# Kernel tuning notes

Hardware: AMD Instinct MI355X
Metric: run time of the kernel (lower is better)

The kernel has to match this reference:

```python
import jax, jax.numpy as jnp
import numpy as np

TAU = 0.75

def normalize_W(W):
    n = jnp.linalg.norm(W)
    n = jax.nn.relu(n - 1.0) + 1.0
    return W / n

def setup_inputs() -> dict:
    key = jax.random.key(0)
    ks = jax.random.split(key, 14)
    C_in, C_out, K = 64, 128, 3
    B, L = 32, 4096
    nh = 64
    chunk_in_d = C_out * K            # 384
    D = C_in * (K + 2 * (C_out // C_in))  # 448
    r = lambda k, shp, s=1.0: jax.random.normal(k, shp, dtype=jnp.float32) * s
    W = normalize_W(r(ks[4], (D, 32)))
    return {
        "x": r(ks[0], (B, C_in, L)),
        "conv_weight": r(ks[1], (C_out, C_in, K), 0.1),
        "bias_param": r(ks[2], (C_out,), 0.1),
        "grads": r(ks[3], (C_out * C_in * K,), 0.1),
        "W": W,
        "ctrl_w": r(ks[5], (nh, chunk_in_d), 0.05),
        "ctrl_b": r(ks[6], (nh,), 0.05),
        "cw_w": r(ks[7], (K, nh), 0.05),
        "cw_b": r(ks[8], (K,), 0.05),
        "cb_w": r(ks[9], (C_out // C_in, nh), 0.05),
        "cb_b": r(ks[10], (C_out // C_in,), 0.05),
        "cf_w": r(ks[11], (C_out // C_in, nh), 0.05),
        "cf_b": r(ks[12], (C_out // C_in,), 0.05),
        "trigger": 1,
    }

def fw_chunks(grads, W, ctrl_w, ctrl_b, cw_w, cw_b, cb_w, cb_b, cf_w, cf_b, trigger, n_chunks):
    g = grads.reshape(n_chunks, -1)                    # (C_in, C_out*K)
    rep = jax.nn.silu(g @ ctrl_w.T + ctrl_b)           # (C_in, nh)
    w = rep @ cw_w.T + cw_b                            # (C_in, K)
    b = rep @ cb_w.T + cb_b                            # (C_in, C_out/C_in)
    f = rep @ cf_w.T + cf_b                            # (C_in, C_out/C_in)
    q = jnp.concatenate([w.ravel(), b.ravel(), f.ravel()])  # (D,)  first call: no q_ema
    W_upd = W
    if trigger == 1:  # codebook attention / top-k / scatter-EMA path
        dim = w.shape[0]
        att = jax.nn.softmax(q @ W / 0.5)              # (32,)
        v, idx = jax.lax.top_k(att, 2)
        ww = W[:, idx]                                 # (D, 2)
        old_w = ww @ idx.astype(jnp.float32)[:, None]  # (D, 1) -- indices used as weights, as in source
        s_att = jnp.zeros((att.shape[0],), jnp.float32).at[idx].set(v)
        W_contrib = old_w @ s_att[None, :]             # (D, 32)
        mask = jnp.ones(W.shape, jnp.float32).at[:, idx].set(TAU)
        W_upd = normalize_W(mask * W + (1.0 - mask) * W_contrib)
        nw, nb, nf = w.shape[1], b.shape[1], f.shape[1]
        o_w = old_w[: nw * dim]
        o_b = old_w[nw * dim : (nw + nb) * dim]
        o_f = old_w[-nf * dim :]
        w = TAU * w + (1.0 - TAU) * o_w.reshape(w.shape)
        b = TAU * b + (1.0 - TAU) * o_b.reshape(b.shape)
        f = TAU * f + (1.0 - TAU) * o_f.reshape(f.shape)
    f = f.reshape(-1)[None, :, None]                   # (1, C_out, 1)
    return w[None], b.reshape(-1), f, W_upd

def reference(x, conv_weight, bias_param, grads, W, ctrl_w, ctrl_b, cw_w, cw_b, cb_w, cb_b, cf_w, cf_b, trigger):
    n_chunks = conv_weight.shape[1]  # in_channels
    w, b, f, W_upd = fw_chunks(grads, W, ctrl_w, ctrl_b, cw_w, cw_b, cb_w, cb_b, cf_w, cf_b, trigger, n_chunks)
    cw = conv_weight * w                               # (C_out, C_in, K)
    pad = ((conv_weight.shape[2] - 1) * 1 + 1) // 2    # receptive_field // 2
    conv_out = jax.lax.conv_general_dilated(
        x, cw, window_strides=(1,), padding=[(pad, pad)], rhs_dilation=(1,),
        dimension_numbers=("NCH", "OIH", "NCH"))
    conv_out = conv_out + (bias_param * b)[None, :, None]
    out = f * conv_out                                 # (B, C_out, L)
    return out, W_upd
```

## Files before the change

kernel.cpp:

```cpp
#include <hip/hip_runtime.h>
#include <hip/hip_bf16.h>
#include <math.h>

#define TAU 0.75f

typedef _Float16 half8 __attribute__((ext_vector_type(8)));
typedef float    f32x4 __attribute__((ext_vector_type(4)));

#define LDS_BARRIER() do {                                   \
    asm volatile("s_waitcnt lgkmcnt(0)" ::: "memory");       \
    __builtin_amdgcn_s_barrier();                            \
    asm volatile("" ::: "memory");                           \
} while (0)

#define SWZ(row) ((((row) >> 3) & 7) << 3)

#define WS_Q     0
#define WS_NORM2 448
#define WS_SCALE 449
#define WS_V01   450
#define WS_I01   452
#define WS_WQ    456
#define WS_FSC   648
#define WS_BADD  776
#define WS_OW    904
#define WS_WF16  1352

__global__ __launch_bounds__(256) void k1_rep_q(
    const float* __restrict__ grads, const float* __restrict__ ctrl_w,
    const float* __restrict__ ctrl_b,
    const float* __restrict__ cw_w, const float* __restrict__ cw_b,
    const float* __restrict__ cb_w, const float* __restrict__ cb_b,
    const float* __restrict__ cf_w, const float* __restrict__ cf_b,
    const float* __restrict__ W, float* __restrict__ ws)
{
    const int t = threadIdx.x;
    if (blockIdx.x == 64) {
        __shared__ float red[256];
        float ss = 0.f;
        for (int e = t; e < 3584; e += 256) {
            const float4 w4 = ((const float4*)W)[e];
            ss += w4.x * w4.x + w4.y * w4.y + w4.z * w4.z + w4.w * w4.w;
        }
        red[t] = ss; __syncthreads();
        for (int s = 128; s > 0; s >>= 1) { if (t < s) red[t] += red[t + s]; __syncthreads(); }
        if (t == 0) ws[WS_NORM2] = red[0];
        return;
    }
    const int c = blockIdx.x;
    __shared__ float gS[384];
    __shared__ float repS[64];
    if (t < 96) ((float4*)gS)[t] = ((const float4*)(grads + c * 384))[t];
    __syncthreads();
    {
        const int h = t >> 2, sub = t & 3;
        const float4* wa = (const float4*)(ctrl_w + h * 384) + sub * 24;
        const float4* ga = (const float4*)gS + sub * 24;
        float dot = 0.f;
        #pragma unroll
        for (int d = 0; d < 24; d++) {
            const float4 a = ga[d], b = wa[d];
            dot += a.x * b.x + a.y * b.y + a.z * b.z + a.w * b.w;
        }
        dot += __shfl_xor(dot, 1);
        dot += __shfl_xor(dot, 2);
        if (sub == 0) {
            const float z = dot + ctrl_b[h];
            repS[h] = z / (1.f + expf(-z));
        }
    }
    __syncthreads();
    if (t < 7) {
        const float* wv; float bias; int e;
        if (t < 3)      { wv = cw_w + t * 64;       bias = cw_b[t];     e = 3 * c + t; }
        else if (t < 5) { const int j = t - 3; wv = cb_w + j * 64; bias = cb_b[j]; e = 192 + 2 * c + j; }
        else            { const int j = t - 5; wv = cf_w + j * 64; bias = cf_b[j]; e = 320 + 2 * c + j; }
        float dot = 0.f;
        #pragma unroll 8
        for (int h = 0; h < 64; h++) dot += repS[h] * wv[h];
        ws[WS_Q + e] = dot + bias;
    }
}

__global__ __launch_bounds__(256) void k2_small(
    const float* __restrict__ W, const float* __restrict__ bias_param,
    const int* __restrict__ trigger, float* __restrict__ ws)
{
    __shared__ float qS[448], owS[448], sS[32], sW[4][32], red[256];
    __shared__ int   idxS[2];
    __shared__ float vS[2];
    const int t = threadIdx.x;
    const int wv = t >> 6, lane = t & 63;
    const int trig = trigger[0];

    for (int e = t; e < 448; e += 256) qS[e] = ws[WS_Q + e];
    __syncthreads();

    {
        const int m = lane & 31, half = lane >> 5;
        float s = 0.f;
        const int base = wv * 112;
        #pragma unroll 4
        for (int it = 0; it < 56; it++) {
            const int d = base + it * 2 + half;
            s += qS[d] * W[d * 32 + m];
        }
        s += __shfl_xor(s, 32);
        if (lane < 32) sW[wv][lane] = s;
    }
    __syncthreads();
    if (t < 32) sS[t] = 2.f * (sW[0][t] + sW[1][t] + sW[2][t] + sW[3][t]);
    __syncthreads();
    if (t == 0) {
        float mx = sS[0];
        for (int m = 1; m < 32; m++) mx = fmaxf(mx, sS[m]);
        float sum = 0.f; float att[32];
        for (int m = 0; m < 32; m++) { att[m] = expf(sS[m] - mx); sum += att[m]; }
        const float inv = 1.f / sum;
        int i0 = 0; float v0 = att[0];
        for (int m = 1; m < 32; m++) if (att[m] > v0) { v0 = att[m]; i0 = m; }
        int i1 = -1; float v1 = -1.f;
        for (int m = 0; m < 32; m++) { if (m == i0) continue; if (att[m] > v1) { v1 = att[m]; i1 = m; } }
        idxS[0] = i0; idxS[1] = i1; vS[0] = v0 * inv; vS[1] = v1 * inv;
    }
    __syncthreads();
    const int i0 = idxS[0], i1 = idxS[1];
    const float v0 = vS[0], v1 = vS[1];

    float corr = 0.f;
    for (int d = t; d < 448; d += 256) {
        const float w0 = W[d * 32 + i0], w1 = W[d * 32 + i1];
        const float ow = (trig == 1) ? (w0 * (float)i0 + w1 * (float)i1) : 0.f;
        owS[d] = ow;
        if (trig == 1) {
            const float n0 = TAU * w0 + 0.25f * ow * v0;
            const float n1 = TAU * w1 + 0.25f * ow * v1;
            corr += n0 * n0 - w0 * w0 + n1 * n1 - w1 * w1;
        }
    }
    red[t] = corr; __syncthreads();
    for (int s = 128; s > 0; s >>= 1) { if (t < s) red[t] += red[t + s]; __syncthreads(); }
    if (t == 0) {
        const float n = sqrtf(fmaxf(ws[WS_NORM2] + red[0], 0.f));
        ws[WS_SCALE] = 1.f / fmaxf(n, 1.f);
        ws[WS_V01] = v0; ws[WS_V01 + 1] = v1;
        ((int*)ws)[WS_I01] = i0; ((int*)ws)[WS_I01 + 1] = i1;
    }

    if (t < 192) ws[WS_WQ + t] = (trig == 1) ? (TAU * qS[t] + 0.25f * owS[t]) : qS[t];
    for (int o = t; o < 128; o += 256) {
        float bb = qS[192 + o], ff = qS[320 + o];
        if (trig == 1) {
            bb = TAU * bb + 0.25f * owS[192 + o];
            ff = TAU * ff + 0.25f * owS[320 + o];
        }
        ws[WS_FSC + o]  = ff;
        ws[WS_BADD + o] = ff * bias_param[o] * bb;
    }
    for (int d = t; d < 448; d += 256) ws[WS_OW + d] = owS[d];
}

__global__ __launch_bounds__(256) void k3_finalize(
    const float* __restrict__ W, const float* __restrict__ conv_weight,
    const int* __restrict__ trigger, const float* __restrict__ ws,
    float* __restrict__ W_out, _Float16* __restrict__ wf_out)
{
    const int g = blockIdx.x * 256 + threadIdx.x;
    const int trig = trigger[0];
    if (g < 14336) {
        const float wv = W[g];
        float wn = wv;
        if (trig == 1) {
            const int d = g >> 5, m = g & 31;
            const int i0 = ((const int*)ws)[WS_I01], i1 = ((const int*)ws)[WS_I01 + 1];
            if (m == i0)      wn = TAU * wv + 0.25f * ws[WS_OW + d] * ws[WS_V01];
            else if (m == i1) wn = TAU * wv + 0.25f * ws[WS_OW + d] * ws[WS_V01 + 1];
            wn *= ws[WS_SCALE];
        }
        W_out[g] = wn;
    } else {
        const int e2 = g - 14336;
        const int o   = e2 / 192;
        const int rem = e2 - o * 192;
        const int i   = rem / 3;
        const int kk  = rem - i * 3;
        wf_out[(kk * 128 + o) * 64 + i] =
            (_Float16)(conv_weight[e2] * ws[WS_WQ + rem] * ws[WS_FSC + o]);
    }
}

__global__ __launch_bounds__(256, 2) void conv_mfma(
    const float* __restrict__ x, const _Float16* __restrict__ wf,
    const float* __restrict__ badd, float* __restrict__ out)
{
    __shared__ __align__(16) _Float16 xs[2][66 * 72];

    const int t     = threadIdx.x;
    const int wv    = t >> 6;
    const int lane  = t & 63;
    const int lrow  = lane & 15;
    const int lgrp  = lane >> 4;
    const int b     = blockIdx.x >> 4;
    const int lbase = (blockIdx.x & 15) * 256;
    const int obase = wv * 32;

    const float* xb = x + (size_t)b * 64 * 4096;
    const int ci = t & 3;
    const int ir = t >> 2;
    const int ei = t & 63;
    const int side = (t >> 6) & 1;

    half8 Wf[2][2][3];
    #pragma unroll
    for (int of = 0; of < 2; of++)
        #pragma unroll
        for (int ch = 0; ch < 2; ch++)
            #pragma unroll
            for (int kk = 0; kk < 3; kk++)
                Wf[of][ch][kk] = *(const half8*)(wf + ((kk * 128 + obase + of * 16 + lrow) * 64 + ch * 32 + lgrp * 8));

    float ba_[2];
    #pragma unroll
    for (int of = 0; of < 2; of++)
        ba_[of] = badd[obase + of * 16 + lrow];

    float4 xrA[4], xrB[4];
    float  xeA = 0.f, xeB = 0.f;

#define STAGE_LOAD(xr, xe, lb) do {                                          \
    _Pragma("unroll")                                                        \
    for (int j = 0; j < 4; j++)                                              \
        (xr)[j] = *(const float4*)(xb + (size_t)ir * 4096 + (lb) + ci * 16 + j * 4); \
    (xe) = 0.f;                                                              \
    if (t < 128) {                                                           \
        const int l_ = side ? ((lb) + 64) : ((lb) - 1);                      \
        if (l_ >= 0 && l_ < 4096) (xe) = xb[(size_t)ei * 4096 + l_];         \
    }                                                                        \
} while (0)

#define STAGE_WRITE(buf, xr, xe) do {                                        \
    _Pragma("unroll")                                                        \
    for (int j = 0; j < 4; j++) {                                            \
        const int r0_ = ci * 16 + j * 4 + 1;                                 \
        (buf)[(r0_ + 0) * 72 + (ir ^ SWZ(r0_ + 0))] = (_Float16)(xr)[j].x;   \
        (buf)[(r0_ + 1) * 72 + (ir ^ SWZ(r0_ + 1))] = (_Float16)(xr)[j].y;   \
        (buf)[(r0_ + 2) * 72 + (ir ^ SWZ(r0_ + 2))] = (_Float16)(xr)[j].z;   \
        (buf)[(r0_ + 3) * 72 + (ir ^ SWZ(r0_ + 3))] = (_Float16)(xr)[j].w;   \
    }                                                                        \
    if (t < 128) {                                                           \
        const int re_ = side ? 65 : 0;                                       \
        (buf)[re_ * 72 + (ei ^ SWZ(re_))] = (_Float16)(xe);                  \
    }                                                                        \
} while (0)

#define COMPUTE_STORE(buf, lb) do {                                          \
    f32x4 acc[2][4];                                                         \
    _Pragma("unroll")                                                        \
    for (int of = 0; of < 2; of++)                                           \
        _Pragma("unroll")                                                    \
        for (int lf = 0; lf < 4; lf++) acc[of][lf] = (f32x4)0.f;             \
    _Pragma("unroll")                                                        \
    for (int ch = 0; ch < 2; ch++) {                                         \
        _Pragma("unroll")                                                    \
        for (int kk = 0; kk < 3; kk++) {                                     \
            half8 Xf[4];                                                     \
            _Pragma("unroll")                                                \
            for (int lf = 0; lf < 4; lf++) {                                 \
                const int rr_ = lf * 16 + lrow + kk;                         \
                Xf[lf] = *(const half8*)((buf) + rr_ * 72 + ((ch * 32 + lgrp * 8) ^ SWZ(rr_))); \
            }                                                                \
            _Pragma("unroll")                                                \
            for (int of = 0; of < 2; of++)                                   \
                _Pragma("unroll")                                            \
                for (int lf = 0; lf < 4; lf++)                               \
                    acc[of][lf] = __builtin_amdgcn_mfma_f32_16x16x32_f16(Xf[lf], Wf[of][ch][kk], acc[of][lf], 0, 0, 0); \
        }                                                                    \
    }                                                                        \
    _Pragma("unroll")                                                        \
    for (int of = 0; of < 2; of++) {                                         \
        const int o_ = obase + of * 16 + lrow;                               \
        float* orow_ = out + ((size_t)(b * 128 + o_)) * 4096 + (lb) + lgrp * 4; \
        _Pragma("unroll")                                                    \
        for (int lf = 0; lf < 4; lf++) {                                     \
            float4 r_;                                                       \
            r_.x = acc[of][lf][0] + ba_[of];                                 \
            r_.y = acc[of][lf][1] + ba_[of];                                 \
            r_.z = acc[of][lf][2] + ba_[of];                                 \
            r_.w = acc[of][lf][3] + ba_[of];                                 \
            *(float4*)(orow_ + lf * 16) = r_;                                \
        }                                                                    \
    }                                                                        \
} while (0)

    STAGE_LOAD(xrA, xeA, lbase);
    STAGE_LOAD(xrB, xeB, lbase + 64);
    STAGE_WRITE(xs[0], xrA, xeA);
    LDS_BARRIER();

    STAGE_LOAD(xrA, xeA, lbase + 128);
    COMPUTE_STORE(xs[0], lbase);
    STAGE_WRITE(xs[1], xrB, xeB);
    LDS_BARRIER();

    STAGE_LOAD(xrB, xeB, lbase + 192);
    COMPUTE_STORE(xs[1], lbase + 64);
    STAGE_WRITE(xs[0], xrA, xeA);
    LDS_BARRIER();

    COMPUTE_STORE(xs[0], lbase + 128);
    STAGE_WRITE(xs[1], xrB, xeB);
    LDS_BARRIER();

    COMPUTE_STORE(xs[1], lbase + 192);

#undef STAGE_LOAD
#undef STAGE_WRITE
#undef COMPUTE_STORE
}

extern "C" void kernel_launch(void* const* d_in, const int* in_sizes, int n_in,
                              void* d_out, int out_size, void* d_ws, size_t ws_size,
                              hipStream_t stream) {
    const float* x           = (const float*)d_in[0];
    const float* conv_weight = (const float*)d_in[1];
    const float* bias_param  = (const float*)d_in[2];
    const float* grads       = (const float*)d_in[3];
    const float* W           = (const float*)d_in[4];
    const float* ctrl_w      = (const float*)d_in[5];
    const float* ctrl_b      = (const float*)d_in[6];
    const float* cw_w        = (const float*)d_in[7];
    const float* cw_b        = (const float*)d_in[8];
    const float* cb_w        = (const float*)d_in[9];
    const float* cb_b        = (const float*)d_in[10];
    const float* cf_w        = (const float*)d_in[11];
    const float* cf_b        = (const float*)d_in[12];
    const int*   trigger     = (const int*)d_in[13];

    float* out   = (float*)d_out;
    float* W_out = out + (size_t)32 * 128 * 4096;
    float* ws    = (float*)d_ws;
    _Float16* wfp = (_Float16*)(ws + WS_WF16);
    float* badd  = ws + WS_BADD;

    k1_rep_q<<<65, 256, 0, stream>>>(grads, ctrl_w, ctrl_b, cw_w, cw_b,
                                     cb_w, cb_b, cf_w, cf_b, W, ws);
    k2_small<<<1, 256, 0, stream>>>(W, bias_param, trigger, ws);
    k3_finalize<<<152, 256, 0, stream>>>(W, conv_weight, trigger, ws, W_out, wfp);
    conv_mfma<<<512, 256, 0, stream>>>(x, wfp, badd, out);
}
```

Baseline: 42.62 us.

## Pre-transpose input to fp16 channel-last and stream tiles into LDS

Adds a separate kernel that converts x to fp16 in a padded, swizzled position-major layout stored in workspace. A new conv kernel then loads tiles straight into LDS with global_load_lds and runs MFMA with register-resident weights. It uses smaller blocks and higher occupancy. This aims to cut the in-kernel conversion and transpose cost, but adds an extra full pass over x through global memory. The new path runs only when the workspace is large enough.

Result: slower. 53.04 us (+24.4%).

```diff
diff --git a/kernel.cpp b/kernel.cpp
--- a/kernel.cpp
+++ b/kernel.cpp
@@ -5,7 +5,11 @@
 #define TAU 0.75f
 
 typedef _Float16 half8 __attribute__((ext_vector_type(8)));
+typedef _Float16 half4v __attribute__((ext_vector_type(4)));
 typedef float    f32x4 __attribute__((ext_vector_type(4)));
+
+#define AS1 __attribute__((address_space(1)))
+#define AS3 __attribute__((address_space(3)))
 
 #define LDS_BARRIER() do {                                   \
     asm volatile("s_waitcnt lgkmcnt(0)" ::: "memory");       \
@@ -25,6 +29,8 @@
 #define WS_BADD  776
 #define WS_OW    904
 #define WS_WF16  1352
+#define WS_XT_BYTE 55296ull
+#define WS_XT_NEED (WS_XT_BYTE + 32ull * 4098ull * 128ull)
 
 __global__ __launch_bounds__(256) void k1_rep_q(
     const float* __restrict__ grads, const float* __restrict__ ctrl_w,
@@ -186,6 +192,138 @@
         const int kk  = rem - i * 3;
         wf_out[(kk * 128 + o) * 64 + i] =
             (_Float16)(conv_weight[e2] * ws[WS_WQ + rem] * ws[WS_FSC + o]);
+    }
+}
+
+__global__ __launch_bounds__(256) void xpose_kernel(
+    const float* __restrict__ x, _Float16* __restrict__ xT)
+{
+    __shared__ _Float16 ls[64 * 72];
+    const int t  = threadIdx.x;
+    const int b  = blockIdx.x >> 6;
+    const int lc = blockIdx.x & 63;
+    const int l0 = lc * 64;
+
+    {
+        const int ir = t >> 2, ci = t & 3;
+        const float* xr = x + (size_t)b * 64 * 4096 + (size_t)ir * 4096 + l0 + ci * 16;
+        #pragma unroll
+        for (int j = 0; j < 4; j++) {
+            const float4 v = *(const float4*)(xr + j * 4);
+            half4v h;
+            h[0] = (_Float16)v.x; h[1] = (_Float16)v.y;
+            h[2] = (_Float16)v.z; h[3] = (_Float16)v.w;
+            *(half4v*)&ls[ir * 72 + ci * 16 + j * 4] = h;
+        }
+    }
+    __syncthreads();
+
+    {
+        const int lr = t >> 2, isub = t & 3;
+        const int pr = l0 + lr + 1;
+        half8 lo, hi;
+        #pragma unroll
+        for (int u = 0; u < 8; u++) lo[u] = ls[(isub * 16 + u) * 72 + lr];
+        #pragma unroll
+        for (int u = 0; u < 8; u++) hi[u] = ls[(isub * 16 + 8 + u) * 72 + lr];
+        _Float16* gb = xT + (((size_t)b * 4098 + pr) << 6);
+        const int sw = pr & 7;
+        *(half8*)(gb + (((isub * 2) ^ sw) << 3))     = lo;
+        *(half8*)(gb + (((isub * 2 + 1) ^ sw) << 3)) = hi;
+    }
+
+    if (lc == 0 && t < 8) {
+        half8 z = (half8)(_Float16)0.f;
+        *(half8*)(xT + (((size_t)b * 4098) << 6) + t * 8) = z;
+    }
+    if (lc == 63 && t < 8) {
+        half8 z = (half8)(_Float16)0.f;
+        *(half8*)(xT + (((size_t)b * 4098 + 4097) << 6) + t * 8) = z;
+    }
+}
+
+__global__ __launch_bounds__(256, 4) void conv_gll(
+    const _Float16* __restrict__ xT, const _Float16* __restrict__ wf,
+    const float* __restrict__ badd, float* __restrict__ out)
+{
+    __shared__ __align__(16) _Float16 ldsT[66 * 64];
+
+    const int t    = threadIdx.x;
+    const int wv   = t >> 6;
+    const int lane = t & 63;
+    const int lrow = lane & 15;
+    const int lgrp = lane >> 4;
+    const int b    = blockIdx.x >> 6;
+    const int lc   = blockIdx.x & 63;
+    const int l0   = lc * 64;
+    const int obase = wv * 32;
+
+    half8 Wf[2][2][3];
+    #pragma unroll
+    for (int of = 0; of < 2; of++)
+        #pragma unroll
+        for (int ch = 0; ch < 2; ch++)
+            #pragma unroll
+            for (int kk = 0; kk < 3; kk++)
+                Wf[of][ch][kk] = *(const half8*)(wf + ((kk * 128 + obase + of * 16 + lrow) * 64 + ch * 32 + lgrp * 8));
+
+    float ba_[2];
+    #pragma unroll
+    for (int of = 0; of < 2; of++)
+        ba_[of] = badd[obase + of * 16 + lrow];
+
+    {
+        const char* src = (const char*)xT + (((size_t)b * 4098 + l0) << 7);
+        char* dst = (char*)ldsT;
+        for (int j = wv; j < 8; j += 4)
+            __builtin_amdgcn_global_load_lds(
+                (const AS1 unsigned int*)(src + j * 1024 + lane * 16),
+                (AS3 unsigned int*)(dst + j * 1024), 16, 0, 0);
+        if (wv == 0)
+            __builtin_amdgcn_global_load_lds(
+                (const AS1 unsigned int*)(src + 7424 + lane * 16),
+                (AS3 unsigned int*)(dst + 7424), 16, 0, 0);
+    }
+    __syncthreads();
+
+    f32x4 acc[2][4];
+    #pragma unroll
+    for (int of = 0; of < 2; of++)
+        #pragma unroll
+        for (int lf = 0; lf < 4; lf++) acc[of][lf] = (f32x4)0.f;
+
+    #pragma unroll
+    for (int ch = 0; ch < 2; ch++) {
+        #pragma unroll
+        for (int kk = 0; kk < 3; kk++) {
+            half8 Xf[4];
+            #pragma unroll
+            for (int lf = 0; lf < 4; lf++) {
+                const int r = lf * 16 + lrow + kk;
+                const int g = (ch * 4 + lgrp) ^ (r & 7);
+                Xf[lf] = *(const half8*)(ldsT + r * 64 + g * 8);
+            }
+            #pragma unroll
+            for (int of = 0; of < 2; of++)
+                #pragma unroll
+                for (int lf = 0; lf < 4; lf++)
+                    acc[of][lf] = __builtin_amdgcn_mfma_f32_16x16x32_f16(Xf[lf], Wf[of][ch][kk], acc[of][lf], 0, 0, 0);
+        }
+    }
+
+    #pragma unroll
+    for (int of = 0; of < 2; of++) {
+        const int o = obase + of * 16 + lrow;
+        float* orow = out + ((size_t)(b * 128 + o)) * 4096 + l0 + lgrp * 4;
+        #pragma unroll
+        for (int lf = 0; lf < 4; lf++) {
+            float4 r;
+            r.x = acc[of][lf][0] + ba_[of];
+            r.y = acc[of][lf][1] + ba_[of];
+            r.z = acc[of][lf][2] + ba_[of];
+            r.w = acc[of][lf][3] + ba_[of];
+            *(float4*)(orow + lf * 16) = r;
+        }
     }
 }
 
@@ -342,9 +480,19 @@
     _Float16* wfp = (_Float16*)(ws + WS_WF16);
     float* badd  = ws + WS_BADD;
 
+    const bool big_ws = (ws_size >= WS_XT_NEED);
+    _Float16* xT = (_Float16*)((char*)d_ws + WS_XT_BYTE);
+
+    if (big_ws)
+        xpose_kernel<<<2048, 256, 0, stream>>>(x, xT);
+
     k1_rep_q<<<65, 256, 0, stream>>>(grads, ctrl_w, ctrl_b, cw_w, cw_b,
                                      cb_w, cb_b, cf_w, cf_b, W, ws);
     k2_small<<<1, 256, 0, stream>>>(W, bias_param, trigger, ws);
     k3_finalize<<<152, 256, 0, stream>>>(W, conv_weight, trigger, ws, W_out, wfp);
-    conv_mfma<<<512, 256, 0, stream>>>(x, wfp, badd, out);
-}
+
+    if (big_ws)
+        conv_gll<<<2048, 256, 0, stream>>>(xT, wfp, badd, out);
+    else
+        conv_mfma<<<512, 256, 0, stream>>>(x, wfp, badd, out);
+}
```
